# Optimization experiments

Measured on AMD Instinct MI355X. Metric: run time of the kernel, lower is better.

The kernel has to match this reference:

```python
import jax, jax.numpy as jnp
import numpy as np

IN_CH = 512
HID_CH = 512
NUM_HEADS = HID_CH // 32  # 16 heads, 32 channels each
GN_GROUPS = 32
EPS = 1e-6


def group_norm(x, scale, bias):
    # x: (b, c, t); GroupNorm over (channels-in-group, t)
    b, c, t = x.shape
    xg = x.reshape(b, GN_GROUPS, c // GN_GROUPS, t)
    mean = xg.mean(axis=(2, 3), keepdims=True)
    var = xg.var(axis=(2, 3), keepdims=True)
    xg = (xg - mean) * jax.lax.rsqrt(var + EPS)
    return xg.reshape(b, c, t) * scale[None, :, None] + bias[None, :, None]


def setup_inputs() -> dict:
    key = jax.random.key(0)
    ks = jax.random.split(key, 12)
    b, t = 16, 8192
    s = 0.02
    return {
        "x": jax.random.normal(ks[0], (b, IN_CH, t), dtype=jnp.float32),
        "gn_scale": jnp.ones((IN_CH,), jnp.float32),
        "gn_bias": jnp.zeros((IN_CH,), jnp.float32),
        "wq": jax.random.normal(ks[1], (HID_CH, IN_CH), jnp.float32) * s,
        "bq": jnp.zeros((HID_CH,), jnp.float32),
        "wk": jax.random.normal(ks[2], (HID_CH, IN_CH), jnp.float32) * s,
        "bk": jnp.zeros((HID_CH,), jnp.float32),
        "wv": jax.random.normal(ks[3], (HID_CH, IN_CH), jnp.float32) * s,
        "bv": jnp.zeros((HID_CH,), jnp.float32),
        "wp": jax.random.normal(ks[4], (IN_CH, HID_CH), jnp.float32) * s,
        "bp": jnp.zeros((IN_CH,), jnp.float32),
    }


def reference(x, gn_scale, gn_bias, wq, bq, wk, bk, wv, bv, wp, bp):
    b, _, t = x.shape
    n = NUM_HEADS
    hc = HID_CH // n  # 32 channels per head
    h = group_norm(x, gn_scale, gn_bias)
    # 1x1 conv == channel GEMM: (b,c_in,t) -> (b,c_out,t)
    q = jnp.einsum('oc,bct->bot', wq, h) + bq[None, :, None]
    k = jnp.einsum('oc,bct->bot', wk, h) + bk[None, :, None]
    v = jnp.einsum('oc,bct->bot', wv, h) + bv[None, :, None]
    q = q.reshape(b, n, hc, t)
    k = k.reshape(b, n, hc, t)
    v = v.reshape(b, n, hc, t)
    # q: softmax over channel dim; k: rearranged to (.., t, c), softmax over c
    q = jax.nn.softmax(q, axis=2)          # (b,n,c,t), softmax over c
    k = jax.nn.softmax(k, axis=2)          # softmax over c (dim=-1 after b n t c rearrange)
    w = jnp.einsum('bnct,bndt->bncd', q, k)   # (b,n,c,c) small cxc matrix
    h = jnp.einsum('bncd,bndt->bnct', w, v)   # (b,n,c,t)
    h = h.reshape(b, HID_CH, t)
    out = jnp.einsum('oc,bct->bot', wp, h) + bp[None, :, None]
    return x + out
```

## Files before the change

kernel.cpp:

```cpp
#include <hip/hip_runtime.h>

typedef _Float16 f16;
typedef _Float16 f16x8 __attribute__((ext_vector_type(8)));
typedef float f32x4 __attribute__((ext_vector_type(4)));
typedef float f32x16 __attribute__((ext_vector_type(16)));


__device__ __forceinline__ void gl_lds16(const f16* g, const void* lds) {
    __builtin_amdgcn_global_load_lds((const __attribute__((address_space(1))) void*)g,
                                     (__attribute__((address_space(3))) void*)lds, 16, 0, 0);
}

__global__ __launch_bounds__(256) void k_stats_conv(const float* __restrict__ x, float* __restrict__ stats,
                                                    const float* __restrict__ wq, const float* __restrict__ wk,
                                                    const float* __restrict__ wv,
                                                    f16* __restrict__ Wqkp, f16* __restrict__ WvT) {
    int tid = threadIdx.x;
    if (blockIdx.x >= 512) {
        int idx = (blockIdx.x - 512) * 256 + tid;
        if (idx < 524288) {
            int row = idx >> 9, c = idx & 511;
            int hg = row >> 8, ri = row & 255;
            int hl = ri >> 6, qk = (ri >> 5) & 1, ch = ri & 31;
            int src = (hg * 4 + hl) * 32 + ch;
            Wqkp[idx] = (f16)(qk ? wk[(size_t)src * 512 + c] : wq[(size_t)src * 512 + c]);
        } else if (idx < 786432) {
            int j = idx - 524288;
            int c = j >> 9, e = j & 511;
            WvT[j] = (f16)wv[(size_t)e * 512 + c];
        }
        return;
    }
    const float* base = x + (size_t)blockIdx.x * 16 * 8192;
    float s = 0.f, s2 = 0.f;
    for (int it = 0; it < 128; ++it) {
        f32x4 v = *(const f32x4*)(base + (size_t)(it * 256 + tid) * 4);
#pragma unroll
        for (int j = 0; j < 4; ++j) { s += v[j]; s2 += v[j] * v[j]; }
    }
    __shared__ float rs[256], rq[256];
    rs[tid] = s; rq[tid] = s2;
    __syncthreads();
    for (int off = 128; off > 0; off >>= 1) {
        if (tid < off) { rs[tid] += rs[tid + off]; rq[tid] += rq[tid + off]; }
        __syncthreads();
    }
    if (tid == 0) {
        float mean = rs[0] * (1.f / 131072.f);
        float var  = rq[0] * (1.f / 131072.f) - mean * mean;
        stats[blockIdx.x * 2 + 0] = mean;
        stats[blockIdx.x * 2 + 1] = rsqrtf(var + 1e-6f);
    }
}

__global__ __launch_bounds__(256) void k_gn_apply(const float* __restrict__ x, const float* __restrict__ stats,
                                                  const float* __restrict__ gsc, const float* __restrict__ gbi,
                                                  f16* __restrict__ h) {
    __shared__ f16 ldsT[64][72];
    int tid = threadIdx.x;
    int tt = blockIdx.x & 127, ct = (blockIdx.x >> 7) & 7, b = blockIdx.x >> 10;
    int cc = tid >> 2, tq = tid & 3;
    int c = ct * 64 + cc;
    int g = c >> 4;
    float mean = stats[(b * 32 + g) * 2 + 0];
    float rstd = stats[(b * 32 + g) * 2 + 1];
    float sc = gsc[c] * rstd;
    float bi = gbi[c] - mean * sc;
    const float* xp = x + ((size_t)b * 512 + c) * 8192 + tt * 64 + tq * 16;
#pragma unroll
    for (int q4 = 0; q4 < 4; ++q4) {
        f32x4 v = *(const f32x4*)(xp + q4 * 4);
#pragma unroll
        for (int j = 0; j < 4; ++j) ldsT[tq * 16 + q4 * 4 + j][cc] = (f16)(v[j] * sc + bi);
    }
    __syncthreads();
    int tl = tid >> 2, cq = tid & 3;
    f16x8 v0 = *(const f16x8*)(&ldsT[tl][cq * 16]);
    f16x8 v1 = *(const f16x8*)(&ldsT[tl][cq * 16 + 8]);
    f16* hp = h + ((size_t)b * 8192 + tt * 64 + tl) * 512 + ct * 64 + cq * 16;
    *(f16x8*)(hp) = v0;
    *(f16x8*)(hp + 8) = v1;
}

__device__ __forceinline__ void gemm_core(const f16* __restrict__ Abase, int lda,
                                          const f16* __restrict__ Bbase,
                                          char* smem, int tid, f32x4 acc[4][4]) {
    const int lane = tid & 63, wave = tid >> 6;
    const int wm = wave >> 1, wn = wave & 1;
    char* As = smem;
    char* Bs = smem + 16384;
    const int srow = (lane >> 3);
    const int schunk = (lane & 7) ^ srow;
    for (int kt = 0; kt < 8; ++kt) {
#pragma unroll
        for (int i = 0; i < 4; ++i) {
            int row = (wave * 4 + i) * 8 + srow;
            gl_lds16(Abase + (size_t)row * lda + kt * 64 + schunk * 8, As + (wave * 4 + i) * 1024);
            gl_lds16(Bbase + (size_t)row * 512 + kt * 64 + schunk * 8, Bs + (wave * 4 + i) * 1024);
        }
        __syncthreads();
#pragma unroll
        for (int ks = 0; ks < 2; ++ks) {
            f16x8 af[4], bf[4];
#pragma unroll
            for (int i = 0; i < 4; ++i) {
                int row = wm * 64 + i * 16 + (lane & 15);
                int ch = (ks * 4 + (lane >> 4)) ^ (lane & 7);
                af[i] = *(const f16x8*)(As + row * 128 + ch * 16);
            }
#pragma unroll
            for (int j = 0; j < 4; ++j) {
                int row = wn * 64 + j * 16 + (lane & 15);
                int ch = (ks * 4 + (lane >> 4)) ^ (lane & 7);
                bf[j] = *(const f16x8*)(Bs + row * 128 + ch * 16);
            }
#pragma unroll
            for (int i = 0; i < 4; ++i)
#pragma unroll
                for (int j = 0; j < 4; ++j)
                    acc[i][j] = __builtin_amdgcn_mfma_f32_16x16x32_f16(af[i], bf[j], acc[i][j], 0, 0, 0);
        }
        __syncthreads();
    }
}

__global__ __launch_bounds__(256, 2) void k_qk_w(const f16* __restrict__ h, const f16* __restrict__ Wqkp,
                                                 float* __restrict__ w_part) {
    __shared__ __align__(16) char smem[49152];
    int tid = threadIdx.x, lane = tid & 63, wave = tid >> 6;
    int bid = blockIdx.x;
    int lb = (bid & 7) * 512 + (bid >> 3);
    int batch = lb >> 8;
    int rem = lb & 255;
    int tt = rem >> 2, hg = rem & 3;
    const f16* Abase = Wqkp + (size_t)hg * 256 * 512;
    const f16* Bbase = h + ((size_t)batch * 8192 + (size_t)tt * 128) * 512;
    char* As = smem;
    char* Bs = smem + 32768;
    const int srow = lane >> 3;
    const int schunk = (lane & 7) ^ srow;
    f32x4 acc[4][8];
#pragma unroll
    for (int i = 0; i < 4; ++i)
#pragma unroll
        for (int j = 0; j < 8; ++j) acc[i][j] = (f32x4){0.f, 0.f, 0.f, 0.f};

    for (int kt = 0; kt < 8; ++kt) {
#pragma unroll
        for (int i = 0; i < 8; ++i) {
            int g = wave * 8 + i;
            gl_lds16(Abase + (size_t)(g * 8 + srow) * 512 + kt * 64 + schunk * 8, As + g * 1024);
        }
#pragma unroll
        for (int i = 0; i < 4; ++i) {
            int g = wave * 4 + i;
            gl_lds16(Bbase + (size_t)(g * 8 + srow) * 512 + kt * 64 + schunk * 8, Bs + g * 1024);
        }
        __syncthreads();
#pragma unroll
        for (int ks = 0; ks < 2; ++ks) {
            f16x8 af[4];
#pragma unroll
            for (int i = 0; i < 4; ++i) {
                int row = wave * 64 + i * 16 + (lane & 15);
                int ch = (ks * 4 + (lane >> 4)) ^ (lane & 7);
                af[i] = *(const f16x8*)(As + row * 128 + ch * 16);
            }
#pragma unroll
            for (int j = 0; j < 8; ++j) {
                int row = j * 16 + (lane & 15);
                int ch = (ks * 4 + (lane >> 4)) ^ (lane & 7);
                f16x8 bf = *(const f16x8*)(Bs + row * 128 + ch * 16);
#pragma unroll
                for (int i = 0; i < 4; ++i)
                    acc[i][j] = __builtin_amdgcn_mfma_f32_16x16x32_f16(af[i], bf, acc[i][j], 0, 0, 0);
            }
        }
        __syncthreads();
    }

    f16* qbuf = (f16*)(smem + wave * 9216);
    f16* kbuf = qbuf + 32 * 72;
    f32x16 wacc;
#pragma unroll
    for (int i = 0; i < 16; ++i) wacc[i] = 0.f;

#pragma unroll
    for (int th = 0; th < 2; ++th) {
#pragma unroll
        for (int jl = 0; jl < 4; ++jl) {
            int j = th * 4 + jl;
#pragma unroll
            for (int qk = 0; qk < 2; ++qk) {
                int ib = qk * 2;
                float v0[8];
#pragma unroll
                for (int i2 = 0; i2 < 2; ++i2)
#pragma unroll
                    for (int r = 0; r < 4; ++r) v0[i2 * 4 + r] = acc[ib + i2][j][r];
                float mx = v0[0];
#pragma unroll
                for (int i = 1; i < 8; ++i) mx = fmaxf(mx, v0[i]);
                mx = fmaxf(mx, __shfl_xor(mx, 16));
                mx = fmaxf(mx, __shfl_xor(mx, 32));
                float s = 0.f;
#pragma unroll
                for (int i = 0; i < 8; ++i) { v0[i] = __expf(v0[i] - mx); s += v0[i]; }
                s += __shfl_xor(s, 16);
                s += __shfl_xor(s, 32);
                float inv = 1.f / s;
                f16* dst = qk ? kbuf : qbuf;
                int tcol = jl * 16 + (lane & 15);
#pragma unroll
                for (int i2 = 0; i2 < 2; ++i2)
#pragma unroll
                    for (int r = 0; r < 4; ++r) {
                        int c = i2 * 16 + (lane >> 4) * 4 + r;
                        dst[c * 72 + tcol] = (f16)(v0[i2 * 4 + r] * inv);
                    }
            }
        }
#pragma unroll
        for (int ks = 0; ks < 4; ++ks) {
            f16x8 a  = *(const f16x8*)(qbuf + (lane & 31) * 72 + ks * 16 + (lane >> 5) * 8);
            f16x8 bb = *(const f16x8*)(kbuf + (lane & 31) * 72 + ks * 16 + (lane >> 5) * 8);
            wacc = __builtin_amdgcn_mfma_f32_32x32x16_f16(a, bb, wacc, 0, 0, 0);
        }
    }
    int ghead = hg * 4 + wave;
    float* wpo = w_part + (((size_t)tt * 16 + batch) * 16 + ghead) * 1024;
#pragma unroll
    for (int r = 0; r < 16; ++r) {
        int row = (r & 3) + 8 * (r >> 2) + 4 * (lane >> 5);
        wpo[row * 32 + (lane & 31)] = wacc[r];
    }
}

__global__ __launch_bounds__(256) void k_wreduce(const float* __restrict__ w_part, float* __restrict__ w_red) {
    int blk = blockIdx.x;
    int tid = threadIdx.x;
    f32x4 s = (f32x4){0.f, 0.f, 0.f, 0.f};
    for (int tt = 0; tt < 64; ++tt) {
        f32x4 v = *(const f32x4*)(w_part + ((size_t)tt * 256 + blk) * 1024 + tid * 4);
        s += v;
    }
    *(f32x4*)(w_red + (size_t)blk * 1024 + tid * 4) = s;
}

__global__ __launch_bounds__(256) void k_wpe(const float* __restrict__ w_red, const float* __restrict__ wp,
                                             const float* __restrict__ bv, const float* __restrict__ bp,
                                             f16* __restrict__ wpe, float* __restrict__ bias_p) {
    __shared__ float wl[16384];
    __shared__ float bred[256];
    int tid = threadIdx.x;
    int b = blockIdx.x >> 3, ot = blockIdx.x & 7;
    for (int idx = tid; idx < 16384; idx += 256) wl[idx] = w_red[(size_t)b * 16384 + idx];
    __syncthreads();
    int o = ot * 64 + (tid >> 2);
    int cq = tid & 3;
    float bacc = 0.f;
#pragma unroll
    for (int ng = 0; ng < 4; ++ng) {
        int n = cq * 4 + ng;
        float a[32];
#pragma unroll
        for (int d = 0; d < 32; ++d) a[d] = 0.f;
        for (int e = 0; e < 32; ++e) {
            float wv = wp[(size_t)o * 512 + n * 32 + e];
#pragma unroll
            for (int d = 0; d < 32; ++d) a[d] += wv * wl[n * 1024 + e * 32 + d];
        }
#pragma unroll
        for (int dc = 0; dc < 4; ++dc) {
            f16x8 o8;
#pragma unroll
            for (int j = 0; j < 8; ++j) o8[j] = (f16)a[dc * 8 + j];
            *(f16x8*)(wpe + ((size_t)b * 512 + o) * 512 + n * 32 + dc * 8) = o8;
        }
#pragma unroll
        for (int d = 0; d < 32; ++d) bacc += a[d] * bv[n * 32 + d];
    }
    bred[tid] = bacc;
    __syncthreads();
    if ((tid & 3) == 0)
        bias_p[(size_t)b * 512 + o] = bp[o] + bred[tid] + bred[tid + 1] + bred[tid + 2] + bred[tid + 3];
}

__global__ __launch_bounds__(256) void k_wfin(const f16* __restrict__ wpe, const f16* __restrict__ WvT,
                                              f16* __restrict__ Wfin) {
    __shared__ __align__(16) char smem[34816];
    int tid = threadIdx.x, lane = tid & 63, wave = tid >> 6;
    int wm = wave >> 1, wn = wave & 1;
    int bid = blockIdx.x;
    int b = bid >> 4, mt = (bid >> 2) & 3, nt = bid & 3;
    const f16* Abase = wpe + (size_t)b * 262144 + (size_t)mt * 128 * 512;
    const f16* Bbase = WvT + (size_t)nt * 128 * 512;
    f32x4 acc[4][4];
#pragma unroll
    for (int i = 0; i < 4; ++i)
#pragma unroll
        for (int j = 0; j < 4; ++j) acc[i][j] = (f32x4){0.f, 0.f, 0.f, 0.f};
    gemm_core(Abase, 512, Bbase, smem, tid, acc);
    f16* epi = (f16*)smem;
#pragma unroll
    for (int i = 0; i < 4; ++i)
#pragma unroll
        for (int j = 0; j < 4; ++j)
#pragma unroll
            for (int r = 0; r < 4; ++r) {
                int m = wm * 64 + i * 16 + (lane >> 4) * 4 + r;
                int n = wn * 64 + j * 16 + (lane & 15);
                epi[m * 136 + n] = (f16)acc[i][j][r];
            }
    __syncthreads();
#pragma unroll
    for (int rr = 0; rr < 8; ++rr) {
        int row = wave * 32 + (lane >> 4) * 8 + rr;
        f16x8 vv = *(const f16x8*)(epi + row * 136 + (lane & 15) * 8);
        *(f16x8*)(Wfin + (size_t)b * 262144 + (size_t)(mt * 128 + row) * 512 + nt * 128 + (lane & 15) * 8) = vv;
    }
}

__global__ __launch_bounds__(256, 2) void k_out(const f16* __restrict__ h, const f16* __restrict__ Wfin,
                                                const float* __restrict__ x, const float* __restrict__ bias_p,
                                                float* __restrict__ out) {
    __shared__ __align__(16) char smem[49152];
    int tid = threadIdx.x, lane = tid & 63, wave = tid >> 6;
    int bid = blockIdx.x;
    int lb = (bid & 7) * 256 + (bid >> 3);
    int batch = lb >> 7;
    int rem = lb & 127;
    int tt = rem >> 1, ot2 = rem & 1;
    const f16* Abase = Wfin + (size_t)batch * 262144 + (size_t)ot2 * 256 * 512;
    const f16* Bbase = h + ((size_t)batch * 8192 + (size_t)tt * 128) * 512;
    char* As = smem;
    char* Bs = smem + 32768;
    const int srow = lane >> 3;
    const int schunk = (lane & 7) ^ srow;
    f32x4 acc[4][8];
#pragma unroll
    for (int i = 0; i < 4; ++i)
#pragma unroll
        for (int j = 0; j < 8; ++j) acc[i][j] = (f32x4){0.f, 0.f, 0.f, 0.f};

    for (int kt = 0; kt < 8; ++kt) {
#pragma unroll
        for (int i = 0; i < 8; ++i) {
            int g = wave * 8 + i;
            gl_lds16(Abase + (size_t)(g * 8 + srow) * 512 + kt * 64 + schunk * 8, As + g * 1024);
        }
#pragma unroll
        for (int i = 0; i < 4; ++i) {
            int g = wave * 4 + i;
            gl_lds16(Bbase + (size_t)(g * 8 + srow) * 512 + kt * 64 + schunk * 8, Bs + g * 1024);
        }
        __syncthreads();
#pragma unroll
        for (int ks = 0; ks < 2; ++ks) {
            f16x8 af[4];
#pragma unroll
            for (int i = 0; i < 4; ++i) {
                int row = wave * 64 + i * 16 + (lane & 15);
                int ch = (ks * 4 + (lane >> 4)) ^ (lane & 7);
                af[i] = *(const f16x8*)(As + row * 128 + ch * 16);
            }
#pragma unroll
            for (int j = 0; j < 8; ++j) {
                int row = j * 16 + (lane & 15);
                int ch = (ks * 4 + (lane >> 4)) ^ (lane & 7);
                f16x8 bf = *(const f16x8*)(Bs + row * 128 + ch * 16);
#pragma unroll
                for (int i = 0; i < 4; ++i)
                    acc[i][j] = __builtin_amdgcn_mfma_f32_16x16x32_f16(af[i], bf, acc[i][j], 0, 0, 0);
            }
        }
        __syncthreads();
    }

    float* ep = (float*)smem;
    const int orow_in = (lane >> 4) * 4;
    for (int ow = 0; ow < 4; ++ow) {
        __syncthreads();
        if (wave == ow) {
#pragma unroll
            for (int i = 0; i < 4; ++i)
#pragma unroll
                for (int j = 0; j < 8; ++j)
#pragma unroll
                    for (int r = 0; r < 4; ++r)
                        ep[(i * 16 + orow_in + r) * 132 + j * 16 + (lane & 15)] = acc[i][j][r];
        }
        __syncthreads();
        int o_g0 = ot2 * 256 + ow * 64;
#pragma unroll
        for (int p = 0; p < 8; ++p) {
            int idx = p * 256 + tid;
            int row = idx >> 5;
            int tq = (idx & 31) * 4;
            int o = o_g0 + row;
            float bpv = bias_p[batch * 512 + o];
            size_t g = ((size_t)batch * 512 + o) * 8192 + (size_t)tt * 128 + tq;
            f32x4 xv = *(const f32x4*)(x + g);
            f32x4 lv = *(const f32x4*)(ep + row * 132 + tq);
            f32x4 ov;
#pragma unroll
            for (int j = 0; j < 4; ++j) ov[j] = xv[j] + bpv + lv[j];
            *(f32x4*)(out + g) = ov;
        }
    }
}

extern "C" void kernel_launch(void* const* d_in, const int* in_sizes, int n_in,
                              void* d_out, int out_size, void* d_ws, size_t ws_size,
                              hipStream_t stream) {
    const float* x   = (const float*)d_in[0];
    const float* gsc = (const float*)d_in[1];
    const float* gbi = (const float*)d_in[2];
    const float* wq  = (const float*)d_in[3];
    const float* bq  = (const float*)d_in[4];  (void)bq;
    const float* wk  = (const float*)d_in[5];
    const float* bk  = (const float*)d_in[6];  (void)bk;
    const float* wv  = (const float*)d_in[7];
    const float* bv  = (const float*)d_in[8];
    const float* wp  = (const float*)d_in[9];
    const float* bp  = (const float*)d_in[10];
    float* out = (float*)d_out;
    char* ws = (char*)d_ws;

    size_t o_stats = 0;
    size_t o_wqkp  = 4096;
    size_t o_wvt   = o_wqkp + 1048576;
    size_t o_biasp = o_wvt + 524288;
    size_t o_wred  = o_biasp + 32768;
    size_t o_wpe   = o_wred + 1048576;
    size_t o_wfin  = o_wpe + 8388608;
    size_t o_wpart = o_wfin + 8388608;
    size_t o_h     = o_wpart + 67108864;
    size_t total   = o_h + 134217728;
    if (ws_size < total) return;

    float* stats  = (float*)(ws + o_stats);
    f16*   Wqkp   = (f16*)(ws + o_wqkp);
    f16*   WvT    = (f16*)(ws + o_wvt);
    float* bias_p = (float*)(ws + o_biasp);
    float* w_red  = (float*)(ws + o_wred);
    f16*   wpe    = (f16*)(ws + o_wpe);
    f16*   Wfin   = (f16*)(ws + o_wfin);
    float* w_part = (float*)(ws + o_wpart);
    f16*   h      = (f16*)(ws + o_h);

    k_stats_conv<<<3584, 256, 0, stream>>>(x, stats, wq, wk, wv, Wqkp, WvT);
    k_gn_apply  <<<16384, 256, 0, stream>>>(x, stats, gsc, gbi, h);
    k_qk_w      <<<4096,  256, 0, stream>>>(h, Wqkp, w_part);
    k_wreduce   <<<256,   256, 0, stream>>>(w_part, w_red);
    k_wpe       <<<128,   256, 0, stream>>>(w_red, wp, bv, bp, wpe, bias_p);
    k_wfin      <<<256,   256, 0, stream>>>(wpe, WvT, Wfin);
    k_out       <<<2048,  256, 0, stream>>>(h, Wfin, x, bias_p, out);
}
```

Before: 530.8 us.

## Fold GroupNorm affine into per-batch weights and compute stats during transpose

Removes the separate full pass over x for GroupNorm statistics. Group sums are now accumulated while x is transposed to fp16, and the normalization scale and shift are folded algebraically into per-batch q/k weights, bias vectors and the final fused weight. This avoids reading x twice, at the cost of building per-batch Wqkp matrices and a small single-block reduction kernel. It also feeds raw un-normalized x in fp16 into the GEMMs, which may change precision.

After: 517.8 us. 1.03x faster.

```diff
diff --git a/kernel.cpp b/kernel.cpp
--- a/kernel.cpp
+++ b/kernel.cpp
@@ -11,75 +11,112 @@
                                      (__attribute__((address_space(3))) void*)lds, 16, 0, 0);
 }
 
-__global__ __launch_bounds__(256) void k_stats_conv(const float* __restrict__ x, float* __restrict__ stats,
-                                                    const float* __restrict__ wq, const float* __restrict__ wk,
-                                                    const float* __restrict__ wv,
-                                                    f16* __restrict__ Wqkp, f16* __restrict__ WvT) {
+__global__ __launch_bounds__(256) void k_tr(const float* __restrict__ x, f16* __restrict__ xT,
+                                            float* __restrict__ part,
+                                            const float* __restrict__ wv, f16* __restrict__ WvT) {
     int tid = threadIdx.x;
-    if (blockIdx.x >= 512) {
-        int idx = (blockIdx.x - 512) * 256 + tid;
-        if (idx < 524288) {
-            int row = idx >> 9, c = idx & 511;
-            int hg = row >> 8, ri = row & 255;
-            int hl = ri >> 6, qk = (ri >> 5) & 1, ch = ri & 31;
-            int src = (hg * 4 + hl) * 32 + ch;
-            Wqkp[idx] = (f16)(qk ? wk[(size_t)src * 512 + c] : wq[(size_t)src * 512 + c]);
-        } else if (idx < 786432) {
-            int j = idx - 524288;
-            int c = j >> 9, e = j & 511;
-            WvT[j] = (f16)wv[(size_t)e * 512 + c];
-        }
+    if (blockIdx.x >= 16384) {
+        int idx = (blockIdx.x - 16384) * 256 + tid;
+        int c = idx >> 9, e = idx & 511;
+        WvT[idx] = (f16)wv[(size_t)e * 512 + c];
         return;
     }
-    const float* base = x + (size_t)blockIdx.x * 16 * 8192;
-    float s = 0.f, s2 = 0.f;
-    for (int it = 0; it < 128; ++it) {
-        f32x4 v = *(const f32x4*)(base + (size_t)(it * 256 + tid) * 4);
-#pragma unroll
-        for (int j = 0; j < 4; ++j) { s += v[j]; s2 += v[j] * v[j]; }
-    }
-    __shared__ float rs[256], rq[256];
-    rs[tid] = s; rq[tid] = s2;
-    __syncthreads();
-    for (int off = 128; off > 0; off >>= 1) {
-        if (tid < off) { rs[tid] += rs[tid + off]; rq[tid] += rq[tid + off]; }
-        __syncthreads();
-    }
-    if (tid == 0) {
-        float mean = rs[0] * (1.f / 131072.f);
-        float var  = rq[0] * (1.f / 131072.f) - mean * mean;
-        stats[blockIdx.x * 2 + 0] = mean;
-        stats[blockIdx.x * 2 + 1] = rsqrtf(var + 1e-6f);
-    }
-}
-
-__global__ __launch_bounds__(256) void k_gn_apply(const float* __restrict__ x, const float* __restrict__ stats,
-                                                  const float* __restrict__ gsc, const float* __restrict__ gbi,
-                                                  f16* __restrict__ h) {
     __shared__ f16 ldsT[64][72];
-    int tid = threadIdx.x;
     int tt = blockIdx.x & 127, ct = (blockIdx.x >> 7) & 7, b = blockIdx.x >> 10;
     int cc = tid >> 2, tq = tid & 3;
     int c = ct * 64 + cc;
-    int g = c >> 4;
-    float mean = stats[(b * 32 + g) * 2 + 0];
-    float rstd = stats[(b * 32 + g) * 2 + 1];
-    float sc = gsc[c] * rstd;
-    float bi = gbi[c] - mean * sc;
     const float* xp = x + ((size_t)b * 512 + c) * 8192 + tt * 64 + tq * 16;
+    float s = 0.f, s2 = 0.f;
 #pragma unroll
     for (int q4 = 0; q4 < 4; ++q4) {
         f32x4 v = *(const f32x4*)(xp + q4 * 4);
 #pragma unroll
-        for (int j = 0; j < 4; ++j) ldsT[tq * 16 + q4 * 4 + j][cc] = (f16)(v[j] * sc + bi);
+        for (int j = 0; j < 4; ++j) {
+            ldsT[tq * 16 + q4 * 4 + j][cc] = (f16)v[j];
+            s += v[j]; s2 += v[j] * v[j];
+        }
+    }
+#pragma unroll
+    for (int k = 1; k < 64; k <<= 1) { s += __shfl_xor(s, k); s2 += __shfl_xor(s2, k); }
+    if ((tid & 63) == 0) {
+        float* pp = part + (((size_t)b * 32 + ct * 4 + (tid >> 6)) * 128 + tt) * 2;
+        pp[0] = s; pp[1] = s2;
     }
     __syncthreads();
     int tl = tid >> 2, cq = tid & 3;
     f16x8 v0 = *(const f16x8*)(&ldsT[tl][cq * 16]);
     f16x8 v1 = *(const f16x8*)(&ldsT[tl][cq * 16 + 8]);
-    f16* hp = h + ((size_t)b * 8192 + tt * 64 + tl) * 512 + ct * 64 + cq * 16;
+    f16* hp = xT + ((size_t)b * 8192 + tt * 64 + tl) * 512 + ct * 64 + cq * 16;
     *(f16x8*)(hp) = v0;
     *(f16x8*)(hp + 8) = v1;
+}
+
+__global__ __launch_bounds__(512) void k_stats2(const float* __restrict__ part, float* __restrict__ stats) {
+    int i = threadIdx.x;
+    const float* pp = part + (size_t)i * 256;
+    float s = 0.f, s2 = 0.f;
+    for (int t = 0; t < 128; ++t) { s += pp[t * 2]; s2 += pp[t * 2 + 1]; }
+    float mean = s * (1.f / 131072.f);
+    float var  = s2 * (1.f / 131072.f) - mean * mean;
+    stats[i * 2 + 0] = mean;
+    stats[i * 2 + 1] = rsqrtf(var + 1e-6f);
+}
+
+__global__ __launch_bounds__(256) void k_prep(const float* __restrict__ wq, const float* __restrict__ wk,
+                                              const float* __restrict__ wv,
+                                              const float* __restrict__ gsc, const float* __restrict__ gbi,
+                                              const float* __restrict__ stats,
+                                              const float* __restrict__ bq, const float* __restrict__ bk,
+                                              f16* __restrict__ Wqkp2, float* __restrict__ qkb,
+                                              float* __restrict__ u) {
+    __shared__ float scn[512], bi[512], red[256];
+    int tid = threadIdx.x;
+    int blk = blockIdx.x;
+    int b = (blk < 256) ? (blk >> 4) : ((blk - 256) >> 3);
+    for (int i = tid; i < 512; i += 256) {
+        float mean = stats[(b * 32 + (i >> 4)) * 2 + 0];
+        float rstd = stats[(b * 32 + (i >> 4)) * 2 + 1];
+        float sc = gsc[i] * rstd;
+        scn[i] = sc;
+        bi[i] = gbi[i] - mean * sc;
+    }
+    __syncthreads();
+    if (blk < 256) {
+        int rg = blk & 15;
+        int pr = rg * 64 + (tid >> 2);
+        int cq = tid & 3;
+        int hg = pr >> 8, ri = pr & 255;
+        int hl = ri >> 6, qk = (ri >> 5) & 1, ch = ri & 31;
+        int src = (hg * 4 + hl) * 32 + ch;
+        const float* wrow = (qk ? wk : wq) + (size_t)src * 512;
+        f16* orow = Wqkp2 + ((size_t)b * 1024 + pr) * 512;
+        float dot = 0.f;
+        for (int c0 = cq * 128; c0 < cq * 128 + 128; c0 += 8) {
+            f16x8 o8;
+#pragma unroll
+            for (int j = 0; j < 8; ++j) {
+                float wv_ = wrow[c0 + j] * scn[c0 + j];
+                o8[j] = (f16)wv_;
+                dot += wv_ * bi[c0 + j];
+            }
+            *(f16x8*)(orow + c0) = o8;
+        }
+        red[tid] = dot;
+        __syncthreads();
+        if (cq == 0)
+            qkb[(size_t)b * 1024 + pr] = red[tid] + red[tid + 1] + red[tid + 2] + red[tid + 3]
+                                         + (qk ? bk[src] : bq[src]);
+    } else {
+        int ug = (blk - 256) & 7;
+        int e = ug * 64 + (tid >> 2);
+        int cq = tid & 3;
+        const float* wrow = wv + (size_t)e * 512;
+        float dot = 0.f;
+        for (int c = cq * 128; c < cq * 128 + 128; ++c) dot += wrow[c] * bi[c];
+        red[tid] = dot;
+        __syncthreads();
+        if (cq == 0) u[(size_t)b * 512 + e] = red[tid] + red[tid + 1] + red[tid + 2] + red[tid + 3];
+    }
 }
 
 __device__ __forceinline__ void gemm_core(const f16* __restrict__ Abase, int lda,
@@ -124,8 +161,8 @@
     }
 }
 
-__global__ __launch_bounds__(256, 2) void k_qk_w(const f16* __restrict__ h, const f16* __restrict__ Wqkp,
-                                                 float* __restrict__ w_part) {
+__global__ __launch_bounds__(256, 2) void k_qk_w(const f16* __restrict__ xT, const f16* __restrict__ Wqkp2,
+                                                 const float* __restrict__ qkb, float* __restrict__ w_part) {
     __shared__ __align__(16) char smem[49152];
     int tid = threadIdx.x, lane = tid & 63, wave = tid >> 6;
     int bid = blockIdx.x;
@@ -133,8 +170,8 @@
     int batch = lb >> 8;
     int rem = lb & 255;
     int tt = rem >> 2, hg = rem & 3;
-    const f16* Abase = Wqkp + (size_t)hg * 256 * 512;
-    const f16* Bbase = h + ((size_t)batch * 8192 + (size_t)tt * 128) * 512;
+    const f16* Abase = Wqkp2 + ((size_t)batch * 1024 + hg * 256) * 512;
+    const f16* Bbase = xT + ((size_t)batch * 8192 + (size_t)tt * 128) * 512;
     char* As = smem;
     char* Bs = smem + 32768;
     const int srow = lane >> 3;
@@ -179,6 +216,15 @@
         __syncthreads();
     }
 
+    float qb[2][8];
+#pragma unroll
+    for (int qk = 0; qk < 2; ++qk)
+#pragma unroll
+        for (int i2 = 0; i2 < 2; ++i2)
+#pragma unroll
+            for (int r = 0; r < 4; ++r)
+                qb[qk][i2 * 4 + r] = qkb[(size_t)batch * 1024 + hg * 256 + wave * 64 + qk * 32 +
+                                         i2 * 16 + (lane >> 4) * 4 + r];
     f16* qbuf = (f16*)(smem + wave * 9216);
     f16* kbuf = qbuf + 32 * 72;
     f32x16 wacc;
@@ -197,7 +243,8 @@
 #pragma unroll
                 for (int i2 = 0; i2 < 2; ++i2)
 #pragma unroll
-                    for (int r = 0; r < 4; ++r) v0[i2 * 4 + r] = acc[ib + i2][j][r];
+                    for (int r = 0; r < 4; ++r)
+                        v0[i2 * 4 + r] = acc[ib + i2][j][r] + qb[qk][i2 * 4 + r];
                 float mx = v0[0];
 #pragma unroll
                 for (int i = 1; i < 8; ++i) mx = fmaxf(mx, v0[i]);
@@ -248,7 +295,8 @@
 }
 
 __global__ __launch_bounds__(256) void k_wpe(const float* __restrict__ w_red, const float* __restrict__ wp,
-                                             const float* __restrict__ bv, const float* __restrict__ bp,
+                                             const float* __restrict__ bv, const float* __restrict__ u,
+                                             const float* __restrict__ bp,
                                              f16* __restrict__ wpe, float* __restrict__ bias_p) {
     __shared__ float wl[16384];
     __shared__ float bred[256];
@@ -278,7 +326,7 @@
             *(f16x8*)(wpe + ((size_t)b * 512 + o) * 512 + n * 32 + dc * 8) = o8;
         }
 #pragma unroll
-        for (int d = 0; d < 32; ++d) bacc += a[d] * bv[n * 32 + d];
+        for (int d = 0; d < 32; ++d) bacc += a[d] * (bv[n * 32 + d] + u[(size_t)b * 512 + n * 32 + d]);
     }
     bred[tid] = bacc;
     __syncthreads();
@@ -287,6 +335,7 @@
 }
 
 __global__ __launch_bounds__(256) void k_wfin(const f16* __restrict__ wpe, const f16* __restrict__ WvT,
+                                              const float* __restrict__ gsc, const float* __restrict__ stats,
                                               f16* __restrict__ Wfin) {
     __shared__ __align__(16) char smem[34816];
     int tid = threadIdx.x, lane = tid & 63, wave = tid >> 6;
@@ -301,6 +350,12 @@
 #pragma unroll
         for (int j = 0; j < 4; ++j) acc[i][j] = (f32x4){0.f, 0.f, 0.f, 0.f};
     gemm_core(Abase, 512, Bbase, smem, tid, acc);
+    float scnj[4];
+#pragma unroll
+    for (int j = 0; j < 4; ++j) {
+        int col = nt * 128 + wn * 64 + j * 16 + (lane & 15);
+        scnj[j] = gsc[col] * stats[(b * 32 + (col >> 4)) * 2 + 1];
+    }
     f16* epi = (f16*)smem;
 #pragma unroll
     for (int i = 0; i < 4; ++i)
@@ -310,7 +365,7 @@
             for (int r = 0; r < 4; ++r) {
                 int m = wm * 64 + i * 16 + (lane >> 4) * 4 + r;
                 int n = wn * 64 + j * 16 + (lane & 15);
-                epi[m * 136 + n] = (f16)acc[i][j][r];
+                epi[m * 136 + n] = (f16)(acc[i][j][r] * scnj[j]);
             }
     __syncthreads();
 #pragma unroll
@@ -321,7 +376,7 @@
     }
 }
 
-__global__ __launch_bounds__(256, 2) void k_out(const f16* __restrict__ h, const f16* __restrict__ Wfin,
+__global__ __launch_bounds__(256, 2) void k_out(const f16* __restrict__ xT, const f16* __restrict__ Wfin,
                                                 const float* __restrict__ x, const float* __restrict__ bias_p,
                                                 float* __restrict__ out) {
     __shared__ __align__(16) char smem[49152];
@@ -332,7 +387,7 @@
     int rem = lb & 127;
     int tt = rem >> 1, ot2 = rem & 1;
     const f16* Abase = Wfin + (size_t)batch * 262144 + (size_t)ot2 * 256 * 512;
-    const f16* Bbase = h + ((size_t)batch * 8192 + (size_t)tt * 128) * 512;
+    const f16* Bbase = xT + ((size_t)batch * 8192 + (size_t)tt * 128) * 512;
     char* As = smem;
     char* Bs = smem + 32768;
     const int srow = lane >> 3;
@@ -417,9 +472,9 @@
     const float* gsc = (const float*)d_in[1];
     const float* gbi = (const float*)d_in[2];
     const float* wq  = (const float*)d_in[3];
-    const float* bq  = (const float*)d_in[4];  (void)bq;
+    const float* bq  = (const float*)d_in[4];
     const float* wk  = (const float*)d_in[5];
-    const float* bk  = (const float*)d_in[6];  (void)bk;
+    const float* bk  = (const float*)d_in[6];
     const float* wv  = (const float*)d_in[7];
     const float* bv  = (const float*)d_in[8];
     const float* wp  = (const float*)d_in[9];
@@ -428,32 +483,39 @@
     char* ws = (char*)d_ws;
 
     size_t o_stats = 0;
-    size_t o_wqkp  = 4096;
-    size_t o_wvt   = o_wqkp + 1048576;
-    size_t o_biasp = o_wvt + 524288;
-    size_t o_wred  = o_biasp + 32768;
+    size_t o_part  = 4096;
+    size_t o_qkb   = o_part + 524288;
+    size_t o_u     = o_qkb + 65536;
+    size_t o_biasp = o_u + 32768;
+    size_t o_wvt   = o_biasp + 32768;
+    size_t o_wred  = o_wvt + 524288;
     size_t o_wpe   = o_wred + 1048576;
     size_t o_wfin  = o_wpe + 8388608;
-    size_t o_wpart = o_wfin + 8388608;
-    size_t o_h     = o_wpart + 67108864;
-    size_t total   = o_h + 134217728;
+    size_t o_wqkp2 = o_wfin + 8388608;
+    size_t o_wpart = o_wqkp2 + 16777216;
+    size_t o_xT    = o_wpart + 67108864;
+    size_t total   = o_xT + 134217728;
     if (ws_size < total) return;
 
     float* stats  = (float*)(ws + o_stats);
-    f16*   Wqkp   = (f16*)(ws + o_wqkp);
+    float* part   = (float*)(ws + o_part);
+    float* qkb    = (float*)(ws + o_qkb);
+    float* u      = (float*)(ws + o_u);
+    float* bias_p = (float*)(ws + o_biasp);
     f16*   WvT    = (f16*)(ws + o_wvt);
-    float* bias_p = (float*)(ws + o_biasp);
     float* w_red  = (float*)(ws + o_wred);
     f16*   wpe    = (f16*)(ws + o_wpe);
     f16*   Wfin   = (f16*)(ws + o_wfin);
+    f16*   Wqkp2  = (f16*)(ws + o_wqkp2);
     float* w_part = (float*)(ws + o_wpart);
-    f16*   h      = (f16*)(ws + o_h);
-
-    k_stats_conv<<<3584, 256, 0, stream>>>(x, stats, wq, wk, wv, Wqkp, WvT);
-    k_gn_apply  <<<16384, 256, 0, stream>>>(x, stats, gsc, gbi, h);
-    k_qk_w      <<<4096,  256, 0, stream>>>(h, Wqkp, w_part);
-    k_wreduce   <<<256,   256, 0, stream>>>(w_part, w_red);
-    k_wpe       <<<128,   256, 0, stream>>>(w_red, wp, bv, bp, wpe, bias_p);
-    k_wfin      <<<256,   256, 0, stream>>>(wpe, WvT, Wfin);
-    k_out       <<<2048,  256, 0, stream>>>(h, Wfin, x, bias_p, out);
-}
+    f16*   xT     = (f16*)(ws + o_xT);
+
+    k_tr     <<<17408, 256, 0, stream>>>(x, xT, part, wv, WvT);
+    k_stats2 <<<1,     512, 0, stream>>>(part, stats);
+    k_prep   <<<384,   256, 0, stream>>>(wq, wk, wv, gsc, gbi, stats, bq, bk, Wqkp2, qkb, u);
+    k_qk_w   <<<4096,  256, 0, stream>>>(xT, Wqkp2, qkb, w_part);
+    k_wreduce<<<256,   256, 0, stream>>>(w_part, w_red);
+    k_wpe    <<<128,   256, 0, stream>>>(w_red, wp, bv, u, bp, wpe, bias_p);
+    k_wfin   <<<256,   256, 0, stream>>>(wpe, WvT, gsc, stats, Wfin);
+    k_out    <<<2048,  256, 0, stream>>>(xT, Wfin, x, bias_p, out);
+}
```
